# Optimization experiments

Hardware: AMD Instinct MI355X
Metric: run time of the kernel (lower is better)

The kernel has to match this reference:

```python
import jax, jax.numpy as jnp
import numpy as np

POOLED_H = 7
POOLED_W = 7
SPATIAL_SCALE = 0.0625


def setup_inputs() -> dict:
    key = jax.random.key(0)
    kf, kb, kc = jax.random.split(key, 3)
    B, C, H, W = 2, 256, 100, 100
    N = 256
    features = jax.random.normal(kf, (B, C, H, W), jnp.float32)
    batch_idx = jax.random.randint(kb, (N,), 0, B).astype(jnp.float32)
    img = H / SPATIAL_SCALE  # image-space extent (1600)
    c = jax.random.uniform(kc, (N, 4), jnp.float32, 0.0, img - 32.0)
    x1 = jnp.minimum(c[:, 0], c[:, 2])
    x2 = jnp.maximum(c[:, 0], c[:, 2]) + 16.0
    y1 = jnp.minimum(c[:, 1], c[:, 3])
    y2 = jnp.maximum(c[:, 1], c[:, 3]) + 16.0
    rois = jnp.stack([batch_idx, x1, y1, x2, y2], axis=1)
    return {"features": features, "rois": rois}


def _hat_cdf(u):
    # antiderivative of the unit hat function phi(u)=max(0,1-|u|), Phi(-inf)=0
    return jnp.where(
        u <= 0.0,
        0.5 * jnp.clip(u + 1.0, 0.0, 1.0) ** 2,
        1.0 - 0.5 * jnp.clip(1.0 - u, 0.0, 1.0) ** 2,
    )


def _bin_weights(lo, hi, size):
    # lo, hi: [N, P] bin boundaries in feature coords -> weights [N, P, size]
    # w[n,p,j] = integral over [lo,hi] of the linear-interp hat centered at j
    idx = jnp.arange(size, dtype=lo.dtype)
    return _hat_cdf(hi[..., None] - idx) - _hat_cdf(lo[..., None] - idx)


def reference(features, rois):
    # Precise RoI Pooling: exact integral of the bilinearly interpolated
    # feature map over each bin, divided by the bin area. Bilinear interp is
    # a tensor product of 1D hats, so the 2D integral separates:
    #   out[n,c,p,q] = (1/area) * sum_{h,w} F[bi,c,h,w] * wy[n,p,h] * wx[n,q,w]
    B, C, H, W = features.shape
    N = rois.shape[0]
    bi = rois[:, 0].astype(jnp.int32)
    x1 = rois[:, 1] * SPATIAL_SCALE
    y1 = rois[:, 2] * SPATIAL_SCALE
    x2 = rois[:, 3] * SPATIAL_SCALE
    y2 = rois[:, 4] * SPATIAL_SCALE
    bw = (x2 - x1) / POOLED_W
    bh = (y2 - y1) / POOLED_H
    ph = jnp.arange(POOLED_H, dtype=rois.dtype)
    pw = jnp.arange(POOLED_W, dtype=rois.dtype)
    ylo = y1[:, None] + ph * bh[:, None]
    yhi = ylo + bh[:, None]
    xlo = x1[:, None] + pw * bw[:, None]
    xhi = xlo + bw[:, None]
    wy = _bin_weights(ylo, yhi, H)  # [N, P, H]
    wx = _bin_weights(xlo, xhi, W)  # [N, Q, W]
    out = jnp.zeros((N, C, POOLED_H, POOLED_W), features.dtype)
    for b in range(B):  # small fixed loop over batch images
        wyb = wy * (bi == b).astype(wy.dtype)[:, None, None]
        out = out + jnp.einsum('chw,nph,nqw->ncpq', features[b], wyb, wx)
    area = jnp.maximum(bw * bh, 0.0)
    out = jnp.where(
        area[:, None, None, None] > 0,
        out / jnp.maximum(area, 1e-12)[:, None, None, None],
        0.0,
    )
    return out
```

## Files before the change

### kernel.cpp

```cpp
#include <hip/hip_runtime.h>
#include <hip/hip_bf16.h>

#define POOLED 7
#define PP 49
#define SCALE 0.0625f
#define WMAX 104
#define RMAX 20
#define TW 256

__device__ __forceinline__ float hat_cdf(float u) {
  if (u <= 0.0f) {
    float t = fminf(fmaxf(u + 1.0f, 0.0f), 1.0f);
    return 0.5f * t * t;
  } else {
    float t = fminf(fmaxf(1.0f - u, 0.0f), 1.0f);
    return 1.0f - 0.5f * t * t;
  }
}

__device__ __forceinline__ float bf_lo(uint32_t u) { return __uint_as_float(u << 16); }
__device__ __forceinline__ float bf_hi(uint32_t u) { return __uint_as_float(u & 0xffff0000u); }

#define FMA4(A, U, WT) do { \
  (A)[0] = fmaf(bf_lo((U).x), (WT), (A)[0]); (A)[1] = fmaf(bf_hi((U).x), (WT), (A)[1]); \
  (A)[2] = fmaf(bf_lo((U).y), (WT), (A)[2]); (A)[3] = fmaf(bf_hi((U).y), (WT), (A)[3]); \
} while (0)

__global__ __launch_bounds__(256)
void transpose_bf16_kernel(const float* __restrict__ in,
                           __hip_bfloat16* __restrict__ out, int C, int S) {
  __shared__ float tile[32][33];
  int b  = blockIdx.z;
  int s0 = blockIdx.x * 32;
  int c0 = blockIdx.y * 32;
  const float* inb = in + (size_t)b * C * S;
  __hip_bfloat16* outb = out + (size_t)b * S * C;
  int tx = threadIdx.x, ty = threadIdx.y;
#pragma unroll
  for (int j = 0; j < 4; j++) {
    int c = c0 + ty + j * 8, s = s0 + tx;
    tile[ty + j * 8][tx] = (c < C && s < S) ? inb[(size_t)c * S + s] : 0.0f;
  }
  __syncthreads();
#pragma unroll
  for (int j = 0; j < 4; j++) {
    int s = s0 + ty + j * 8, c = c0 + tx;
    if (s < S && c < C) outb[(size_t)s * C + c] = __float2bfloat16(tile[tx][ty + j * 8]);
  }
}

__global__ __launch_bounds__(TW, 4)
void prroi_kernel(const __hip_bfloat16* __restrict__ ft,
                  const float* __restrict__ rois,
                  float* __restrict__ out, int N, int C, int H, int W) {
  __shared__ float s_wx[4 * WMAX];
  __shared__ float s_wy[RMAX];
  __shared__ float s_red[4 * 64 * 17];

  const int PG = POOLED * 2;
  int nb = gridDim.x;
  int bid = blockIdx.x;
  if ((nb & 7) == 0) {
    int cpx = nb >> 3;
    bid = (bid & 7) * cpx + (bid >> 3);
  }
  int n = bid / PG;
  int r = bid - n * PG;
  int p = r >> 1;
  int half = r & 1;
  int qlo = half ? 4 : 0;
  int qn  = half ? 3 : 4;

  int tid = threadIdx.x;
  int wave = tid >> 6, lane = tid & 63;

  float bif = rois[n * 5 + 0];
  float x1  = rois[n * 5 + 1] * SCALE;
  float y1  = rois[n * 5 + 2] * SCALE;
  float x2  = rois[n * 5 + 3] * SCALE;
  float y2  = rois[n * 5 + 4] * SCALE;
  int bi = (int)bif;
  float bw = (x2 - x1) * (1.0f / POOLED);
  float bh = (y2 - y1) * (1.0f / POOLED);
  float ylo = y1 + p * bh, yhi = ylo + bh;

  int w0 = max(0, (int)floorf(x1));
  int w1 = min(W - 1, (int)ceilf(x2));
  int nw = w1 - w0 + 1;
  int h0 = max(0, (int)floorf(ylo));
  int h1 = min(H - 1, (int)ceilf(yhi));
  int rows = h1 - h0 + 1;
  if (rows > RMAX) rows = RMAX;

  float area = fmaxf(bw * bh, 0.0f);
  float inv_area = (area > 0.0f) ? 1.0f / fmaxf(area, 1e-12f) : 0.0f;

  for (int i = tid; i < 4 * WMAX; i += TW) {
    int jj = i / WMAX, iw = i - jj * WMAX;
    int q = qlo + jj;
    float v = 0.0f;
    if (iw < nw && q < POOLED) {
      float lo = x1 + q * bw, hi = lo + bw;
      float j = (float)(w0 + iw);
      v = (hat_cdf(hi - j) - hat_cdf(lo - j)) * inv_area;
    }
    s_wx[i] = v;
  }
  for (int i = tid; i < rows; i += TW) {
    float j = (float)(h0 + i);
    s_wy[i] = hat_cdf(yhi - j) - hat_cdf(ylo - j);
  }
  __syncthreads();

  int qa[4], qb[4];
#pragma unroll
  for (int jj = 0; jj < 4; jj++) {
    if (jj < qn) {
      int q = qlo + jj;
      float lo = x1 + q * bw, hi = lo + bw;
      qa[jj] = max(0, (int)floorf(lo) - w0);
      qb[jj] = min(nw - 1, (int)ceilf(hi) - w0);
    } else {
      qa[jj] = 1; qb[jj] = 0;
    }
  }

  float acc[4][4];
#pragma unroll
  for (int jj = 0; jj < 4; jj++)
#pragma unroll
    for (int k = 0; k < 4; k++) acc[jj][k] = 0.0f;

  const int C4 = C >> 2;
  const uint2* lp = (const uint2*)ft + ((size_t)bi * H * W) * C4 + lane;

  for (int ih = wave; ih < rows; ih += 8) {
    int iA = ih, iB = ih + 4;
    float wyA = s_wy[iA];
    float wyB = (iB < rows) ? s_wy[iB] : 0.0f;
    if (wyA == 0.0f && wyB == 0.0f) continue;
    if (wyA == 0.0f) { wyA = wyB; wyB = 0.0f; iA = iB; }
    bool bOK = (wyB != 0.0f);

    const uint2* rpA = lp + (size_t)((h0 + iA) * W + w0) * C4;
    const uint2* rpB = bOK ? lp + (size_t)((h0 + iB) * W + w0) * C4 : rpA;

#pragma unroll
    for (int jj = 0; jj < 4; jj++) {
      int a = qa[jj], b = qb[jj];
      const float* wq = s_wx + jj * WMAX;
      int iw = a;
      if (bOK) {
        for (; iw + 3 <= b; iw += 4) {
          float wx0 = wq[iw], wx1 = wq[iw + 1], wx2 = wq[iw + 2], wx3 = wq[iw + 3];
          uint2 uA0 = rpA[(size_t)iw * C4];
          uint2 uA1 = rpA[(size_t)(iw + 1) * C4];
          uint2 uA2 = rpA[(size_t)(iw + 2) * C4];
          uint2 uA3 = rpA[(size_t)(iw + 3) * C4];
          uint2 uB0 = rpB[(size_t)iw * C4];
          uint2 uB1 = rpB[(size_t)(iw + 1) * C4];
          uint2 uB2 = rpB[(size_t)(iw + 2) * C4];
          uint2 uB3 = rpB[(size_t)(iw + 3) * C4];
          FMA4(acc[jj], uA0, wyA * wx0); FMA4(acc[jj], uA1, wyA * wx1);
          FMA4(acc[jj], uA2, wyA * wx2); FMA4(acc[jj], uA3, wyA * wx3);
          FMA4(acc[jj], uB0, wyB * wx0); FMA4(acc[jj], uB1, wyB * wx1);
          FMA4(acc[jj], uB2, wyB * wx2); FMA4(acc[jj], uB3, wyB * wx3);
        }
        for (; iw <= b; iw++) {
          float wx0 = wq[iw];
          uint2 uA = rpA[(size_t)iw * C4];
          uint2 uB = rpB[(size_t)iw * C4];
          FMA4(acc[jj], uA, wyA * wx0);
          FMA4(acc[jj], uB, wyB * wx0);
        }
      } else {
        for (; iw + 3 <= b; iw += 4) {
          float wx0 = wq[iw], wx1 = wq[iw + 1], wx2 = wq[iw + 2], wx3 = wq[iw + 3];
          uint2 uA0 = rpA[(size_t)iw * C4];
          uint2 uA1 = rpA[(size_t)(iw + 1) * C4];
          uint2 uA2 = rpA[(size_t)(iw + 2) * C4];
          uint2 uA3 = rpA[(size_t)(iw + 3) * C4];
          FMA4(acc[jj], uA0, wyA * wx0); FMA4(acc[jj], uA1, wyA * wx1);
          FMA4(acc[jj], uA2, wyA * wx2); FMA4(acc[jj], uA3, wyA * wx3);
        }
        for (; iw <= b; iw++) {
          float wx0 = wq[iw];
          uint2 uA = rpA[(size_t)iw * C4];
          FMA4(acc[jj], uA, wyA * wx0);
        }
      }
    }
  }

  float* slot = s_red + (size_t)(wave * 64 + lane) * 17;
#pragma unroll
  for (int jj = 0; jj < 4; jj++)
#pragma unroll
    for (int k = 0; k < 4; k++) slot[jj * 4 + k] = acc[jj][k];
  __syncthreads();

  for (int i = tid; i < 256 * 4; i += TW) {
    int c = i >> 2, jj = i & 3;
    if (jj >= qn) continue;
    int base = (c >> 2) * 17 + jj * 4 + (c & 3);
    float v = s_red[base] + s_red[base + 64 * 17] +
              s_red[base + 2 * 64 * 17] + s_red[base + 3 * 64 * 17];
    out[((size_t)n * C + c) * PP + p * POOLED + qlo + jj] = v;
  }
}

__global__ void prroi_fallback(const float* __restrict__ feat,
                               const float* __restrict__ rois,
                               float* __restrict__ out, int N, int C, int H, int W) {
  int idx = blockIdx.x * blockDim.x + threadIdx.x;
  if (idx >= N * C * PP) return;
  int n = idx / (C * PP), r = idx % (C * PP);
  int c = r / PP, pq = r % PP;
  int p = pq / POOLED, q = pq % POOLED;
  float x1 = rois[n * 5 + 1] * SCALE, y1 = rois[n * 5 + 2] * SCALE;
  float x2 = rois[n * 5 + 3] * SCALE, y2 = rois[n * 5 + 4] * SCALE;
  int bi = (int)rois[n * 5 + 0];
  float bw = (x2 - x1) / POOLED, bh = (y2 - y1) / POOLED;
  float xlo = x1 + q * bw, xhi = xlo + bw;
  float ylo = y1 + p * bh, yhi = ylo + bh;
  float area = fmaxf(bw * bh, 0.0f);
  float inv_area = (area > 0.0f) ? 1.0f / fmaxf(area, 1e-12f) : 0.0f;
  const float* f = feat + ((size_t)bi * C + c) * H * W;
  float acc = 0.0f;
  int h0 = max(0, (int)floorf(ylo)), h1 = min(H - 1, (int)ceilf(yhi));
  int w0 = max(0, (int)floorf(xlo)), w1 = min(W - 1, (int)ceilf(xhi));
  for (int h = h0; h <= h1; h++) {
    float wy = hat_cdf(yhi - h) - hat_cdf(ylo - h);
    for (int w = w0; w <= w1; w++) {
      float wx = hat_cdf(xhi - w) - hat_cdf(xlo - w);
      acc += f[h * W + w] * wy * wx;
    }
  }
  out[idx] = acc * inv_area;
}

extern "C" void kernel_launch(void* const* d_in, const int* in_sizes, int n_in,
                              void* d_out, int out_size, void* d_ws, size_t ws_size,
                              hipStream_t stream) {
  const float* feat = (const float*)d_in[0];
  const float* rois = (const float*)d_in[1];
  float* out = (float*)d_out;

  const int B = 2, H = 100, W = 100, S = H * W;
  int N = in_sizes[1] / 5;
  int C = out_size / (N * PP);

  size_t need = (size_t)B * S * C * sizeof(__hip_bfloat16);
  if (C == 256 && ws_size >= need) {
    __hip_bfloat16* ft = (__hip_bfloat16*)d_ws;
    dim3 tb(32, 8);
    dim3 tg((S + 31) / 32, (C + 31) / 32, B);
    transpose_bf16_kernel<<<tg, tb, 0, stream>>>(feat, ft, C, S);
    prroi_kernel<<<N * POOLED * 2, TW, 0, stream>>>(ft, rois, out, N, C, H, W);
  } else {
    int total = N * C * PP;
    prroi_fallback<<<(total + 255) / 256, 256, 0, stream>>>(feat, rois, out, N, C, H, W);
  }
}
```

Measured before the change: 55.44 us.

## Assign one block per output bin instead of per half-row of bins

Changes the work split so each block computes a single (p,q) bin rather than up to four bins of a row half. The grid grows from N*14 to N*49 blocks, each with a smaller wx table, fewer accumulators and a simpler reduction. This aims for more parallelism and less register and LDS pressure per block. The cost is more block launch overhead and loss of reuse, since columns shared by adjacent bins are re-read from the feature map.

Measured after the change: 52.73 us. -4.9%, faster.

```diff
diff --git a/kernel.cpp b/kernel.cpp
--- a/kernel.cpp
+++ b/kernel.cpp
@@ -4,8 +4,8 @@
 #define POOLED 7
 #define PP 49
 #define SCALE 0.0625f
-#define WMAX 104
 #define RMAX 20
+#define QMAX 24
 #define TW 256
 
 __device__ __forceinline__ float hat_cdf(float u) {
@@ -53,23 +53,19 @@
 void prroi_kernel(const __hip_bfloat16* __restrict__ ft,
                   const float* __restrict__ rois,
                   float* __restrict__ out, int N, int C, int H, int W) {
-  __shared__ float s_wx[4 * WMAX];
+  __shared__ float s_wx[QMAX];
   __shared__ float s_wy[RMAX];
-  __shared__ float s_red[4 * 64 * 17];
-
-  const int PG = POOLED * 2;
+  __shared__ float s_red[4 * 64 * 5];
+
   int nb = gridDim.x;
   int bid = blockIdx.x;
   if ((nb & 7) == 0) {
     int cpx = nb >> 3;
     bid = (bid & 7) * cpx + (bid >> 3);
   }
-  int n = bid / PG;
-  int r = bid - n * PG;
-  int p = r >> 1;
-  int half = r & 1;
-  int qlo = half ? 4 : 0;
-  int qn  = half ? 3 : 4;
+  int n = bid / PP;
+  int pq = bid - n * PP;
+  int p = pq / POOLED, q = pq - p * POOLED;
 
   int tid = threadIdx.x;
   int wave = tid >> 6, lane = tid & 63;
@@ -83,28 +79,23 @@
   float bw = (x2 - x1) * (1.0f / POOLED);
   float bh = (y2 - y1) * (1.0f / POOLED);
   float ylo = y1 + p * bh, yhi = ylo + bh;
-
-  int w0 = max(0, (int)floorf(x1));
-  int w1 = min(W - 1, (int)ceilf(x2));
-  int nw = w1 - w0 + 1;
+  float xlo = x1 + q * bw, xhi = xlo + bw;
+
   int h0 = max(0, (int)floorf(ylo));
   int h1 = min(H - 1, (int)ceilf(yhi));
   int rows = h1 - h0 + 1;
   if (rows > RMAX) rows = RMAX;
+  int w0 = max(0, (int)floorf(xlo));
+  int w1 = min(W - 1, (int)ceilf(xhi));
+  int nw = w1 - w0 + 1;
+  if (nw > QMAX) nw = QMAX;
 
   float area = fmaxf(bw * bh, 0.0f);
   float inv_area = (area > 0.0f) ? 1.0f / fmaxf(area, 1e-12f) : 0.0f;
 
-  for (int i = tid; i < 4 * WMAX; i += TW) {
-    int jj = i / WMAX, iw = i - jj * WMAX;
-    int q = qlo + jj;
-    float v = 0.0f;
-    if (iw < nw && q < POOLED) {
-      float lo = x1 + q * bw, hi = lo + bw;
-      float j = (float)(w0 + iw);
-      v = (hat_cdf(hi - j) - hat_cdf(lo - j)) * inv_area;
-    }
-    s_wx[i] = v;
+  for (int i = tid; i < nw; i += TW) {
+    float j = (float)(w0 + i);
+    s_wx[i] = (hat_cdf(xhi - j) - hat_cdf(xlo - j)) * inv_area;
   }
   for (int i = tid; i < rows; i += TW) {
     float j = (float)(h0 + i);
@@ -112,24 +103,7 @@
   }
   __syncthreads();
 
-  int qa[4], qb[4];
-#pragma unroll
-  for (int jj = 0; jj < 4; jj++) {
-    if (jj < qn) {
-      int q = qlo + jj;
-      float lo = x1 + q * bw, hi = lo + bw;
-      qa[jj] = max(0, (int)floorf(lo) - w0);
-      qb[jj] = min(nw - 1, (int)ceilf(hi) - w0);
-    } else {
-      qa[jj] = 1; qb[jj] = 0;
-    }
-  }
-
-  float acc[4][4];
-#pragma unroll
-  for (int jj = 0; jj < 4; jj++)
-#pragma unroll
-    for (int k = 0; k < 4; k++) acc[jj][k] = 0.0f;
+  float acc[4] = {0.0f, 0.0f, 0.0f, 0.0f};
 
   const int C4 = C >> 2;
   const uint2* lp = (const uint2*)ft + ((size_t)bi * H * W) * C4 + lane;
@@ -145,68 +119,58 @@
     const uint2* rpA = lp + (size_t)((h0 + iA) * W + w0) * C4;
     const uint2* rpB = bOK ? lp + (size_t)((h0 + iB) * W + w0) * C4 : rpA;
 
+    int iw = 0;
+    if (bOK) {
+      for (; iw + 3 < nw; iw += 4) {
+        float wx0 = s_wx[iw], wx1 = s_wx[iw + 1], wx2 = s_wx[iw + 2], wx3 = s_wx[iw + 3];
+        uint2 uA0 = rpA[(size_t)iw * C4];
+        uint2 uA1 = rpA[(size_t)(iw + 1) * C4];
+        uint2 uA2 = rpA[(size_t)(iw + 2) * C4];
+        uint2 uA3 = rpA[(size_t)(iw + 3) * C4];
+        uint2 uB0 = rpB[(size_t)iw * C4];
+        uint2 uB1 = rpB[(size_t)(iw + 1) * C4];
+        uint2 uB2 = rpB[(size_t)(iw + 2) * C4];
+        uint2 uB3 = rpB[(size_t)(iw + 3) * C4];
+        FMA4(acc, uA0, wyA * wx0); FMA4(acc, uA1, wyA * wx1);
+        FMA4(acc, uA2, wyA * wx2); FMA4(acc, uA3, wyA * wx3);
+        FMA4(acc, uB0, wyB * wx0); FMA4(acc, uB1, wyB * wx1);
+        FMA4(acc, uB2, wyB * wx2); FMA4(acc, uB3, wyB * wx3);
+      }
+      for (; iw < nw; iw++) {
+        float wx0 = s_wx[iw];
+        uint2 uA = rpA[(size_t)iw * C4];
+        uint2 uB = rpB[(size_t)iw * C4];
+        FMA4(acc, uA, wyA * wx0);
+        FMA4(acc, uB, wyB * wx0);
+      }
+    } else {
+      for (; iw + 3 < nw; iw += 4) {
+        float wx0 = s_wx[iw], wx1 = s_wx[iw + 1], wx2 = s_wx[iw + 2], wx3 = s_wx[iw + 3];
+        uint2 uA0 = rpA[(size_t)iw * C4];
+        uint2 uA1 = rpA[(size_t)(iw + 1) * C4];
+        uint2 uA2 = rpA[(size_t)(iw + 2) * C4];
+        uint2 uA3 = rpA[(size_t)(iw + 3) * C4];
+        FMA4(acc, uA0, wyA * wx0); FMA4(acc, uA1, wyA * wx1);
+        FMA4(acc, uA2, wyA * wx2); FMA4(acc, uA3, wyA * wx3);
+      }
+      for (; iw < nw; iw++) {
+        float wx0 = s_wx[iw];
+        uint2 uA = rpA[(size_t)iw * C4];
+        FMA4(acc, uA, wyA * wx0);
+      }
+    }
+  }
+
+  float* slot = s_red + (size_t)(wave * 64 + lane) * 5;
 #pragma unroll
-    for (int jj = 0; jj < 4; jj++) {
-      int a = qa[jj], b = qb[jj];
-      const float* wq = s_wx + jj * WMAX;
-      int iw = a;
-      if (bOK) {
-        for (; iw + 3 <= b; iw += 4) {
-          float wx0 = wq[iw], wx1 = wq[iw + 1], wx2 = wq[iw + 2], wx3 = wq[iw + 3];
-          uint2 uA0 = rpA[(size_t)iw * C4];
-          uint2 uA1 = rpA[(size_t)(iw + 1) * C4];
-          uint2 uA2 = rpA[(size_t)(iw + 2) * C4];
-          uint2 uA3 = rpA[(size_t)(iw + 3) * C4];
-          uint2 uB0 = rpB[(size_t)iw * C4];
-          uint2 uB1 = rpB[(size_t)(iw + 1) * C4];
-          uint2 uB2 = rpB[(size_t)(iw + 2) * C4];
-          uint2 uB3 = rpB[(size_t)(iw + 3) * C4];
-          FMA4(acc[jj], uA0, wyA * wx0); FMA4(acc[jj], uA1, wyA * wx1);
-          FMA4(acc[jj], uA2, wyA * wx2); FMA4(acc[jj], uA3, wyA * wx3);
-          FMA4(acc[jj], uB0, wyB * wx0); FMA4(acc[jj], uB1, wyB * wx1);
-          FMA4(acc[jj], uB2, wyB * wx2); FMA4(acc[jj], uB3, wyB * wx3);
-        }
-        for (; iw <= b; iw++) {
-          float wx0 = wq[iw];
-          uint2 uA = rpA[(size_t)iw * C4];
-          uint2 uB = rpB[(size_t)iw * C4];
-          FMA4(acc[jj], uA, wyA * wx0);
-          FMA4(acc[jj], uB, wyB * wx0);
-        }
-      } else {
-        for (; iw + 3 <= b; iw += 4) {
-          float wx0 = wq[iw], wx1 = wq[iw + 1], wx2 = wq[iw + 2], wx3 = wq[iw + 3];
-          uint2 uA0 = rpA[(size_t)iw * C4];
-          uint2 uA1 = rpA[(size_t)(iw + 1) * C4];
-          uint2 uA2 = rpA[(size_t)(iw + 2) * C4];
-          uint2 uA3 = rpA[(size_t)(iw + 3) * C4];
-          FMA4(acc[jj], uA0, wyA * wx0); FMA4(acc[jj], uA1, wyA * wx1);
-          FMA4(acc[jj], uA2, wyA * wx2); FMA4(acc[jj], uA3, wyA * wx3);
-        }
-        for (; iw <= b; iw++) {
-          float wx0 = wq[iw];
-          uint2 uA = rpA[(size_t)iw * C4];
-          FMA4(acc[jj], uA, wyA * wx0);
-        }
-      }
-    }
-  }
-
-  float* slot = s_red + (size_t)(wave * 64 + lane) * 17;
-#pragma unroll
-  for (int jj = 0; jj < 4; jj++)
-#pragma unroll
-    for (int k = 0; k < 4; k++) slot[jj * 4 + k] = acc[jj][k];
+  for (int k = 0; k < 4; k++) slot[k] = acc[k];
   __syncthreads();
 
-  for (int i = tid; i < 256 * 4; i += TW) {
-    int c = i >> 2, jj = i & 3;
-    if (jj >= qn) continue;
-    int base = (c >> 2) * 17 + jj * 4 + (c & 3);
-    float v = s_red[base] + s_red[base + 64 * 17] +
-              s_red[base + 2 * 64 * 17] + s_red[base + 3 * 64 * 17];
-    out[((size_t)n * C + c) * PP + p * POOLED + qlo + jj] = v;
-  }
+  int c = tid;
+  int base = (c >> 2) * 5 + (c & 3);
+  float v = s_red[base] + s_red[base + 64 * 5] +
+            s_red[base + 2 * 64 * 5] + s_red[base + 3 * 64 * 5];
+  out[((size_t)n * C + c) * PP + pq] = v;
 }
 
 __global__ void prroi_fallback(const float* __restrict__ feat,
@@ -256,7 +220,7 @@
     dim3 tb(32, 8);
     dim3 tg((S + 31) / 32, (C + 31) / 32, B);
     transpose_bf16_kernel<<<tg, tb, 0, stream>>>(feat, ft, C, S);
-    prroi_kernel<<<N * POOLED * 2, TW, 0, stream>>>(ft, rois, out, N, C, H, W);
+    prroi_kernel<<<N * PP, TW, 0, stream>>>(ft, rois, out, N, C, H, W);
   } else {
     int total = N * C * PP;
     prroi_fallback<<<(total + 255) / 256, 256, 0, stream>>>(feat, rois, out, N, C, H, W);
```
